# Kernel tuning notes

Hardware: AMD Instinct MI355X
Metric: run time of the kernel (lower is better)

Reference implementation:

```python
import jax, jax.numpy as jnp
import numpy as np

B, T, H, IN = 256, 1024, 512, 1

def setup_inputs() -> dict:
    key = jax.random.key(0)
    ks = jax.random.split(key, 10)
    s = 1.0 / np.sqrt(H)
    return {
        "input": jax.random.normal(ks[0], (B, T), dtype=jnp.float32),
        "Wx0": jax.random.uniform(ks[1], (IN, 4 * H), jnp.float32, -s, s),
        "Wh0": jax.random.uniform(ks[2], (H, 4 * H), jnp.float32, -s, s),
        "b0": jax.random.uniform(ks[3], (4 * H,), jnp.float32, -s, s),
        "Wx1": jax.random.uniform(ks[4], (H, 4 * H), jnp.float32, -s, s),
        "Wh1": jax.random.uniform(ks[5], (H, 4 * H), jnp.float32, -s, s),
        "b1": jax.random.uniform(ks[6], (4 * H,), jnp.float32, -s, s),
        "Wf": jax.random.uniform(ks[7], (H, 1), jnp.float32, -s, s),
        "bf": jax.random.uniform(ks[8], (1,), jnp.float32, -s, s),
    }

def _lstm_layer(xs, Wx, Wh, b):
    # xs: [T, B, in] -> hs: [T, B, H]
    Bd = xs.shape[1]
    Hd = Wh.shape[0]
    h0 = jnp.zeros((Bd, Hd), xs.dtype)
    c0 = jnp.zeros((Bd, Hd), xs.dtype)
    def step(carry, x_t):
        h, c = carry
        g = x_t @ Wx + h @ Wh + b                     # [B, 4H]
        i, f, gg, o = jnp.split(g, 4, axis=-1)
        i = jax.nn.sigmoid(i)
        f = jax.nn.sigmoid(f)
        gg = jnp.tanh(gg)
        o = jax.nn.sigmoid(o)
        c_n = f * c + i * gg
        h_n = o * jnp.tanh(c_n)
        return (h_n, c_n), h_n
    _, hs = jax.lax.scan(step, (h0, c0), xs)
    return hs

def reference(input, Wx0, Wh0, b0, Wx1, Wh1, b1, Wf, bf):
    # input: [B, T] scalar sequence (input_size = 1)
    xs = input.T[:, :, None]                           # [T, B, 1]
    h1 = _lstm_layer(xs, Wx0, Wh0, b0)                 # [T, B, H]
    h2 = _lstm_layer(h1, Wx1, Wh1, b1)                 # [T, B, H]
    out = h2 @ Wf + bf                                 # [T, B, 1]
    return out[:, :, 0].T                              # [B, T]
```

## Files before the change

### kernel.cpp

```cpp
#include <hip/hip_runtime.h>


typedef _Float16 f16;
typedef _Float16 f16x8 __attribute__((ext_vector_type(8)));
typedef float f32x4 __attribute__((ext_vector_type(4)));
typedef unsigned long long u64;

#define NB 256
#define NT_ 1024
#define NH 512
#define RING 16
#define SLOT (NB * NH)

__device__ __forceinline__ float sigm(float x)  { return 1.0f / (1.0f + __expf(-x)); }
__device__ __forceinline__ float tanhx(float x) { return 2.0f / (1.0f + __expf(-2.0f * x)) - 1.0f; }

__device__ __forceinline__ void st8(unsigned short* p, u64 v) {
  __hip_atomic_store((u64*)p, v, __ATOMIC_RELAXED, __HIP_MEMORY_SCOPE_AGENT);
}
__device__ __forceinline__ void stf(unsigned* p, unsigned v) {
  __hip_atomic_store(p, v, __ATOMIC_RELAXED, __HIP_MEMORY_SCOPE_AGENT);
}
__device__ __forceinline__ unsigned ldf(const unsigned* p) {
  return __hip_atomic_load(p, __ATOMIC_RELAXED, __HIP_MEMORY_SCOPE_AGENT);
}
__device__ __forceinline__ unsigned pollr(const unsigned* a, unsigned thr) {
  unsigned v;
  for (;;) {
    v = ldf(a);
    if (!~__ballot(v >= thr)) break;
    __builtin_amdgcn_s_sleep(1);
  }
  asm volatile("" ::: "memory");
  return v;
}

__device__ __forceinline__ unsigned* PFL(unsigned* pf, int c, int j, int r) {
  return pf + (((c * 16 + j) * 4) + r) * 32;
}
__device__ __forceinline__ unsigned* QFL(unsigned* qf, int c, int j, int r) {
  return qf + (((c * 32 + j) * 4) + r) * 32;
}

__global__ void prep_xT(const float* __restrict__ inp, float* __restrict__ xT) {
  int g = blockIdx.x * 256 + threadIdx.x;
  int t = g >> 8, b = g & 255;
  xT[t * NB + b] = inp[b * NT_ + t];
}

__global__ void prep_w(const float* __restrict__ Wh0,
                       const float* __restrict__ Wx1,
                       const float* __restrict__ Wh1,
                       f16* __restrict__ dst) {
  int g = blockIdx.x * 256 + threadIdx.x;
  int mat = g >> 20;
  int r = g & 0xFFFFF;
  int j = r & 7, ln = (r >> 3) & 63, kt = (r >> 9) & 15;
  int cl = ln & 15, qd = ln >> 4;
  int k = kt * 32 + qd * 8 + j;
  size_t di; int gcol; const float* W;
  if (mat == 0) {
    int gt = (r >> 13) & 3, nh = (r >> 15) & 1, sl = (r >> 16) & 15;
    W = Wh0;
    gcol = gt * 512 + sl * 32 + nh * 16 + cl;
    di = (size_t)sl * 65536 + (((size_t)(nh * 4 + gt) * 16 + kt) * 64 + ln) * 8 + j;
  } else {
    int jt = (r >> 13) & 1, nh = (r >> 14) & 1, sl = (r >> 15) & 31;
    W = (mat == 1) ? Wx1 : Wh1;
    int gate = jt * 2 + (cl >> 3);
    gcol = gate * 512 + sl * 16 + nh * 8 + (cl & 7);
    di = (size_t)mat * 1048576 + (size_t)sl * 32768 +
         (((size_t)(nh * 2 + jt) * 16 + kt) * 64 + ln) * 8 + j;
  }
  dst[di] = (f16)W[(size_t)k * 2048 + gcol];
}

__global__ void reduce_out(const float* __restrict__ part8,
                           const float* __restrict__ bfp,
                           float* __restrict__ out) {
  int g = blockIdx.x * 256 + threadIdx.x;
  float v = bfp[0];
#pragma unroll
  for (int j = 0; j < 8; ++j) v += part8[(size_t)j * (NB * NT_) + g];
  out[g] = v;
}

__global__ __launch_bounds__(256, 1) void lstm_main(
    const float* __restrict__ xT,
    const f16*  __restrict__ wsl,
    const float* __restrict__ wx0,
    const float* __restrict__ bias0,
    const float* __restrict__ bias1,
    const float* __restrict__ wf,
    unsigned short* p_hi, unsigned short* p_lo,
    unsigned short* q_hi, unsigned short* q_lo,
    unsigned int* pf,
    unsigned int* qf,
    float* part8)
{
  extern __shared__ char smem[];
  const int tid = threadIdx.x;
  const int wv = tid >> 6, ln = tid & 63;
  const int qd = ln >> 4, cl = ln & 15;
  const int bx = blockIdx.x;
  const int r8 = bx & 7, idx = bx >> 3;
  const bool isL0 = !(r8 & 1);
  const int c = r8 >> 1;
  const int sl = idx;
  if (isL0 && idx >= 16) return;
  const float LO = 1.0f / 1024.0f;

  if (isL0) {
    const int4* s0 = (const int4*)wsl + (size_t)sl * 8192;
    int4* d = (int4*)smem;
    for (int i = tid; i < 8192; i += 256) d[i] = s0[i];
  } else {
    const int4* s1 = (const int4*)wsl + 131072 + (size_t)sl * 4096;
    const int4* s2 = (const int4*)wsl + 262144 + (size_t)sl * 4096;
    int4* d = (int4*)smem;
    for (int i = tid; i < 4096; i += 256) { d[i] = s1[i]; d[4096 + i] = s2[i]; }
  }
  __syncthreads();

  if (isL0) {
    const int nh = wv >> 1, rhalf = wv & 1;
    const int rb0 = c * 64 + rhalf * 32;
    float wx0v[4], b0c[4];
#pragma unroll
    for (int g = 0; g < 4; ++g) {
      int gc = g * 512 + sl * 32 + nh * 16 + cl;
      wx0v[g] = wx0[gc];
      b0c[g] = bias0[gc];
    }
    float cst[2][4] = {{0.f,0.f,0.f,0.f},{0.f,0.f,0.f,0.f}};
    const bool isq = (ln >= 16 && ln < 48);
    const unsigned* pwa;
    if (ln < 16)      pwa = PFL(pf, c, ln, sl & 3);
    else if (ln < 48) pwa = QFL(qf, c, ln - 16, sl & 3);
    else              pwa = PFL(pf, c, ln - 48, (sl + 1) & 3);
    const f16x8* wl = (const f16x8*)smem;
    f16* sh  = (f16*)(smem + 131072);
    f16* slo = sh + 2048;

    for (int s = 0; s < NT_; ++s) {
      if ((s & (RING - 1)) == 0 && s) {
        __syncthreads();
        if (wv == 0)
          asm volatile("buffer_inv sc1\n\ts_waitcnt vmcnt(0)" ::: "memory");
        __syncthreads();
      }
      const int slot_r = (s + RING - 1) & (RING - 1);
      const int slot_w = s & (RING - 1);
      float4 xv[2];
#pragma unroll
      for (int rt = 0; rt < 2; ++rt)
        xv[rt] = *(const float4*)(xT + s * NB + rb0 + rt * 16 + qd * 4);
      if (s) {
        unsigned thr = isq ? (s >= RING ? (unsigned)(s - RING + 1) : 0u)
                           : (unsigned)s;
        pollr(pwa, thr);
      }
      f16x8 Ah[16][2], Al[16][2];
      {
        const f16* bh = (const f16*)p_hi + (size_t)slot_r * SLOT + (size_t)c * 32768 + qd * 8;
        const f16* bl = (const f16*)p_lo + (size_t)slot_r * SLOT + (size_t)c * 32768 + qd * 8;
#pragma unroll
        for (int kt = 0; kt < 16; ++kt)
#pragma unroll
          for (int rt = 0; rt < 2; ++rt) {
            int lr = rhalf * 32 + rt * 16 + cl;
            size_t off = (size_t)kt * 2048 + lr * 32;
            Ah[kt][rt] = *(const f16x8*)(bh + off);
            Al[kt][rt] = *(const f16x8*)(bl + off);
          }
      }
      f32x4 acc[4][2], accL[4][2];
#pragma unroll
      for (int g = 0; g < 4; ++g)
#pragma unroll
        for (int rt = 0; rt < 2; ++rt) {
          acc[g][rt] = (f32x4){0.f,0.f,0.f,0.f};
          accL[g][rt] = (f32x4){0.f,0.f,0.f,0.f};
        }
#pragma unroll
      for (int kt = 0; kt < 16; ++kt) {
#pragma unroll
        for (int g = 0; g < 4; ++g) {
          f16x8 bw = wl[((nh * 4 + g) * 16 + kt) * 64 + ln];
#pragma unroll
          for (int rt = 0; rt < 2; ++rt) {
            acc[g][rt]  = __builtin_amdgcn_mfma_f32_16x16x32_f16(Ah[kt][rt], bw, acc[g][rt], 0, 0, 0);
            accL[g][rt] = __builtin_amdgcn_mfma_f32_16x16x32_f16(Al[kt][rt], bw, accL[g][rt], 0, 0, 0);
          }
        }
      }
#pragma unroll
      for (int rt = 0; rt < 2; ++rt)
#pragma unroll
        for (int e = 0; e < 4; ++e) {
          float xe = (e == 0) ? xv[rt].x : (e == 1) ? xv[rt].y : (e == 2) ? xv[rt].z : xv[rt].w;
          float gi = acc[0][rt][e] + accL[0][rt][e] * LO + xe * wx0v[0] + b0c[0];
          float gf = acc[1][rt][e] + accL[1][rt][e] * LO + xe * wx0v[1] + b0c[1];
          float gg = acc[2][rt][e] + accL[2][rt][e] * LO + xe * wx0v[2] + b0c[2];
          float go = acc[3][rt][e] + accL[3][rt][e] * LO + xe * wx0v[3] + b0c[3];
          float ii = sigm(gi), ff = sigm(gf), tg = tanhx(gg), oo = sigm(go);
          cst[rt][e] = ff * cst[rt][e] + ii * tg;
          float h = oo * tanhx(cst[rt][e]);
          f16 hh = (f16)h;
          int su = (rhalf * 32 + rt * 16 + qd * 4 + e) * 32 + nh * 16 + cl;
          sh[su]  = hh;
          slo[su] = (f16)((h - (float)hh) * 1024.0f);
        }
      __syncthreads();
      {
        unsigned short* bh = p_hi + (size_t)slot_w * SLOT + (size_t)c * 32768 + (size_t)sl * 2048;
        unsigned short* bl = p_lo + (size_t)slot_w * SLOT + (size_t)c * 32768 + (size_t)sl * 2048;
#pragma unroll
        for (int i = tid; i < 1024; i += 256) {
          int strm = i >> 9, pc = i & 511;
          const f16* src = (strm ? slo : sh) + pc * 4;
          st8((strm ? bl : bh) + pc * 4, *(const u64*)src);
        }
      }
      __syncthreads();
      if (tid < 4)
        stf(PFL(pf, c, sl, tid), (unsigned)(s + 1));
    }
  } else {
    int u = cl & 7, g01 = cl >> 3;
    const bool hiH = (cl < 8);
    float b1c0[2], b1c1[2], wfv[2];
#pragma unroll
    for (int nh = 0; nh < 2; ++nh) {
      int base = sl * 16 + nh * 8 + u;
      b1c0[nh] = bias1[g01 * 512 + base];
      b1c1[nh] = bias1[(2 + g01) * 512 + base];
      wfv[nh] = wf[base];
    }
    const int lr = wv * 16 + cl;
    float cst[2][4] = {{0.f,0.f,0.f,0.f},{0.f,0.f,0.f,0.f}};
    const unsigned* a_init;
    const bool isPf = (ln >= 32 && ln < 48);
    if (ln < 32)      a_init = QFL(qf, c, ln, sl & 3);
    else if (ln < 48) a_init = PFL(pf, c, ln - 32, sl & 3);
    else              a_init = QFL(qf, c, ln - 48, (sl + 1) & 3);
    const unsigned* ppf = PFL(pf, c, ln & 15, (sl + (ln >> 4)) & 3);
    const f16x8* wx_ = (const f16x8*)smem;
    const f16x8* wh_ = (const f16x8*)(smem + 65536);
    f16* sh  = (f16*)(smem + 131072);
    f16* slo = sh + 1024;

    for (int s = 0; s < NT_; ++s) {
      if ((s & (RING - 1)) == 0 && s) {
        __syncthreads();
        if (wv == 0)
          asm volatile("buffer_inv sc1\n\ts_waitcnt vmcnt(0)" ::: "memory");
        __syncthreads();
      }
      const int slot_r = (s + RING - 1) & (RING - 1);
      const int slot_w = s & (RING - 1);
      bool early = false;
      if (s) {
        unsigned thr_i = isPf ? (unsigned)(s + 1) : (unsigned)s;
        unsigned v = ldf(a_init);
        u64 bal = __ballot(v >= thr_i);
        while ((unsigned)bal != 0xFFFFFFFFu) {
          __builtin_amdgcn_s_sleep(1);
          v = ldf(a_init);
          bal = __ballot(v >= thr_i);
        }
        asm volatile("" ::: "memory");
        early = (((bal >> 32) & 0xFFFF) == 0xFFFF);
      }
      const f16* aqh = (const f16*)q_hi + (size_t)slot_r * SLOT + (size_t)c * 32768 +
                       (qd >> 1) * 1024 + lr * 16 + (qd & 1) * 8;
      const f16* aql = (const f16*)q_lo + (size_t)slot_r * SLOT + (size_t)c * 32768 +
                       (qd >> 1) * 1024 + lr * 16 + (qd & 1) * 8;
      f16x8 Aq[16][2];
#pragma unroll
      for (int kt = 0; kt < 16; ++kt) {
        Aq[kt][0] = *(const f16x8*)(aqh + kt * 2048);
        Aq[kt][1] = *(const f16x8*)(aql + kt * 2048);
      }
      const f16* aph = (const f16*)p_hi + (size_t)slot_w * SLOT + (size_t)c * 32768 +
                       lr * 32 + qd * 8;
      const f16* apl = (const f16*)p_lo + (size_t)slot_w * SLOT + (size_t)c * 32768 +
                       lr * 32 + qd * 8;
      f16x8 Ap[16][2];
      if (early) {
#pragma unroll
        for (int kt = 0; kt < 16; ++kt) {
          Ap[kt][0] = *(const f16x8*)(aph + kt * 2048);
          Ap[kt][1] = *(const f16x8*)(apl + kt * 2048);
        }
      }
      f32x4 acc[4], accL[4];
#pragma unroll
      for (int t4 = 0; t4 < 4; ++t4) {
        acc[t4] = (f32x4){0.f,0.f,0.f,0.f};
        accL[t4] = (f32x4){0.f,0.f,0.f,0.f};
      }
#pragma unroll
      for (int kt = 0; kt < 16; ++kt) {
#pragma unroll
        for (int t4 = 0; t4 < 4; ++t4) {
          f16x8 bw = wh_[(t4 * 16 + kt) * 64 + ln];
          acc[t4]  = __builtin_amdgcn_mfma_f32_16x16x32_f16(Aq[kt][0], bw, acc[t4], 0, 0, 0);
          accL[t4] = __builtin_amdgcn_mfma_f32_16x16x32_f16(Aq[kt][1], bw, accL[t4], 0, 0, 0);
        }
      }
      if (!early) {
        pollr(ppf, (unsigned)(s + 1));
#pragma unroll
        for (int kt = 0; kt < 16; ++kt) {
          Ap[kt][0] = *(const f16x8*)(aph + kt * 2048);
          Ap[kt][1] = *(const f16x8*)(apl + kt * 2048);
        }
      }
#pragma unroll
      for (int kt = 0; kt < 16; ++kt) {
#pragma unroll
        for (int t4 = 0; t4 < 4; ++t4) {
          f16x8 bw = wx_[(t4 * 16 + kt) * 64 + ln];
          acc[t4]  = __builtin_amdgcn_mfma_f32_16x16x32_f16(Ap[kt][0], bw, acc[t4], 0, 0, 0);
          accL[t4] = __builtin_amdgcn_mfma_f32_16x16x32_f16(Ap[kt][1], bw, accL[t4], 0, 0, 0);
        }
      }
      float po[4];
#pragma unroll
      for (int e = 0; e < 4; ++e) {
        po[e] = 0.0f;
#pragma unroll
        for (int nh = 0; nh < 2; ++nh) {
          float v0 = acc[nh*2+0][e] + accL[nh*2+0][e] * LO + b1c0[nh];
          float v1 = acc[nh*2+1][e] + accL[nh*2+1][e] * LO + b1c1[nh];
          float w0 = __shfl_xor(v0, 8, 16);
          float w1 = __shfl_xor(v1, 8, 16);
          float gi = hiH ? v0 : w0;
          float gf = hiH ? w0 : v0;
          float gg = hiH ? v1 : w1;
          float go = hiH ? w1 : v1;
          float ii = sigm(gi), ff = sigm(gf), tg = tanhx(gg), oo = sigm(go);
          cst[nh][e] = ff * cst[nh][e] + ii * tg;
          float h = oo * tanhx(cst[nh][e]);
          int su = (wv * 16 + qd * 4 + e) * 16 + nh * 8 + u;
          if (hiH) {
            sh[su] = (f16)h;
          } else {
            f16 hh = (f16)h;
            slo[su] = (f16)((h - (float)hh) * 1024.0f);
          }
          po[e] += hiH ? wfv[nh] * h : 0.0f;
        }
      }
      __syncthreads();
      {
        unsigned short* bhq = q_hi + (size_t)slot_w * SLOT + (size_t)c * 32768 + (size_t)sl * 1024;
        unsigned short* blq = q_lo + (size_t)slot_w * SLOT + (size_t)c * 32768 + (size_t)sl * 1024;
#pragma unroll
        for (int i = tid; i < 512; i += 256) {
          int strm = i >> 8, pc = i & 255;
          const f16* src = (strm ? slo : sh) + pc * 4;
          st8((strm ? blq : bhq) + pc * 4, *(const u64*)src);
        }
      }
      __syncthreads();
      if (tid < 4)
        stf(QFL(qf, c, sl, tid), (unsigned)(s + 1));
#pragma unroll
      for (int e = 0; e < 4; ++e) {
        float r = po[e];
#pragma unroll
        for (int m = 1; m < 16; m <<= 1) r += __shfl_xor(r, m, 16);
        if (cl == 0)
          atomicAdd(part8 + (size_t)(sl & 7) * (NB * NT_) +
                        (size_t)(c * 64 + wv * 16 + qd * 4 + e) * NT_ + s, r);
      }
    }
  }
}

extern "C" void kernel_launch(void* const* d_in, const int* in_sizes, int n_in,
                              void* d_out, int out_size, void* d_ws, size_t ws_size,
                              hipStream_t stream) {
  (void)in_sizes; (void)n_in; (void)out_size; (void)ws_size;
  const float* inp = (const float*)d_in[0];
  const float* Wx0 = (const float*)d_in[1];
  const float* Wh0 = (const float*)d_in[2];
  const float* b0  = (const float*)d_in[3];
  const float* Wx1 = (const float*)d_in[4];
  const float* Wh1 = (const float*)d_in[5];
  const float* b1  = (const float*)d_in[6];
  const float* Wf  = (const float*)d_in[7];
  const float* bf  = (const float*)d_in[8];

  const size_t MB = 1u << 20;
  const size_t OFF_W    = 0;
  const size_t OFF_XT   = 6 * MB;
  const size_t OFF_PHI  = 7 * MB;
  const size_t OFF_PLO  = 11 * MB;
  const size_t OFF_QHI  = 15 * MB;
  const size_t OFF_QLO  = 19 * MB;
  const size_t OFF_PART = 23 * MB;
  const size_t OFF_CTR  = 31 * MB;

  char* ws = (char*)d_ws;
  f16* wsl = (f16*)(ws + OFF_W);
  float* xT = (float*)(ws + OFF_XT);
  unsigned short* phi = (unsigned short*)(ws + OFF_PHI);
  unsigned short* plo = (unsigned short*)(ws + OFF_PLO);
  unsigned short* qhi = (unsigned short*)(ws + OFF_QHI);
  unsigned short* qlo = (unsigned short*)(ws + OFF_QLO);
  float* part8 = (float*)(ws + OFF_PART);
  unsigned int* pfl = (unsigned int*)(ws + OFF_CTR);
  unsigned int* qfl = pfl + 8192;
  float* out = (float*)d_out;

  (void)hipFuncSetAttribute((const void*)lstm_main,
                            hipFuncAttributeMaxDynamicSharedMemorySize, 139264);

  (void)hipMemsetAsync(ws + OFF_PHI, 0, (OFF_CTR + 98304) - OFF_PHI, stream);

  prep_xT<<<1024, 256, 0, stream>>>(inp, xT);
  prep_w<<<12288, 256, 0, stream>>>(Wh0, Wx1, Wh1, wsl);

  lstm_main<<<256, 256, 139264, stream>>>(xT, wsl, Wx0, b0, b1, Wf,
                                          phi, plo, qhi, qlo, pfl, qfl, part8);

  reduce_out<<<1024, 256, 0, stream>>>(part8, bf, out);
}
```

Baseline: 10.21 ms.

## Split layer-0 LSTM across 32 slices per batch chunk instead of 16

```diff
diff --git a/kernel.cpp b/kernel.cpp
--- a/kernel.cpp
+++ b/kernel.cpp
@@ -36,7 +36,7 @@
 }
 
 __device__ __forceinline__ unsigned* PFL(unsigned* pf, int c, int j, int r) {
-  return pf + (((c * 16 + j) * 4) + r) * 32;
+  return pf + (((c * 32 + j) * 4) + r) * 32;
 }
 __device__ __forceinline__ unsigned* QFL(unsigned* qf, int c, int j, int r) {
   return qf + (((c * 32 + j) * 4) + r) * 32;
@@ -58,20 +58,12 @@
   int j = r & 7, ln = (r >> 3) & 63, kt = (r >> 9) & 15;
   int cl = ln & 15, qd = ln >> 4;
   int k = kt * 32 + qd * 8 + j;
-  size_t di; int gcol; const float* W;
-  if (mat == 0) {
-    int gt = (r >> 13) & 3, nh = (r >> 15) & 1, sl = (r >> 16) & 15;
-    W = Wh0;
-    gcol = gt * 512 + sl * 32 + nh * 16 + cl;
-    di = (size_t)sl * 65536 + (((size_t)(nh * 4 + gt) * 16 + kt) * 64 + ln) * 8 + j;
-  } else {
-    int jt = (r >> 13) & 1, nh = (r >> 14) & 1, sl = (r >> 15) & 31;
-    W = (mat == 1) ? Wx1 : Wh1;
-    int gate = jt * 2 + (cl >> 3);
-    gcol = gate * 512 + sl * 16 + nh * 8 + (cl & 7);
-    di = (size_t)mat * 1048576 + (size_t)sl * 32768 +
-         (((size_t)(nh * 2 + jt) * 16 + kt) * 64 + ln) * 8 + j;
-  }
+  int jt = (r >> 13) & 1, nh = (r >> 14) & 1, sl = (r >> 15) & 31;
+  const float* W = (mat == 0) ? Wh0 : (mat == 1) ? Wx1 : Wh1;
+  int gate = jt * 2 + (cl >> 3);
+  int gcol = gate * 512 + sl * 16 + nh * 8 + (cl & 7);
+  size_t di = (size_t)mat * 1048576 + (size_t)sl * 32768 +
+              (((size_t)(nh * 2 + jt) * 16 + kt) * 64 + ln) * 8 + j;
   dst[di] = (f16)W[(size_t)k * 2048 + gcol];
 }
 
@@ -107,13 +99,15 @@
   const bool isL0 = !(r8 & 1);
   const int c = r8 >> 1;
   const int sl = idx;
-  if (isL0 && idx >= 16) return;
   const float LO = 1.0f / 1024.0f;
+  const int u = cl & 7, g01 = cl >> 3;
+  const bool hiH = (cl < 8);
+  const int lr = wv * 16 + cl;
 
   if (isL0) {
-    const int4* s0 = (const int4*)wsl + (size_t)sl * 8192;
+    const int4* s0 = (const int4*)wsl + (size_t)sl * 4096;
     int4* d = (int4*)smem;
-    for (int i = tid; i < 8192; i += 256) d[i] = s0[i];
+    for (int i = tid; i < 4096; i += 256) d[i] = s0[i];
   } else {
     const int4* s1 = (const int4*)wsl + 131072 + (size_t)sl * 4096;
     const int4* s2 = (const int4*)wsl + 262144 + (size_t)sl * 4096;
@@ -123,24 +117,21 @@
   __syncthreads();
 
   if (isL0) {
-    const int nh = wv >> 1, rhalf = wv & 1;
-    const int rb0 = c * 64 + rhalf * 32;
-    float wx0v[4], b0c[4];
-#pragma unroll
-    for (int g = 0; g < 4; ++g) {
-      int gc = g * 512 + sl * 32 + nh * 16 + cl;
-      wx0v[g] = wx0[gc];
-      b0c[g] = bias0[gc];
+    float w0a[2], w0b[2], b0a[2], b0b[2];
+#pragma unroll
+    for (int nh = 0; nh < 2; ++nh) {
+      int base = sl * 16 + nh * 8 + u;
+      w0a[nh] = wx0[g01 * 512 + base];
+      b0a[nh] = bias0[g01 * 512 + base];
+      w0b[nh] = wx0[(2 + g01) * 512 + base];
+      b0b[nh] = bias0[(2 + g01) * 512 + base];
     }
     float cst[2][4] = {{0.f,0.f,0.f,0.f},{0.f,0.f,0.f,0.f}};
-    const bool isq = (ln >= 16 && ln < 48);
-    const unsigned* pwa;
-    if (ln < 16)      pwa = PFL(pf, c, ln, sl & 3);
-    else if (ln < 48) pwa = QFL(qf, c, ln - 16, sl & 3);
-    else              pwa = PFL(pf, c, ln - 48, (sl + 1) & 3);
+    const unsigned* pwa = (ln < 32) ? PFL(pf, c, ln, sl & 3)
+                                    : QFL(qf, c, ln - 32, sl & 3);
     const f16x8* wl = (const f16x8*)smem;
-    f16* sh  = (f16*)(smem + 131072);
-    f16* slo = sh + 2048;
+    f16* sh  = (f16*)(smem + 65536);
+    f16* slo = sh + 1024;
 
     for (int s = 0; s < NT_; ++s) {
       if ((s & (RING - 1)) == 0 && s) {
@@ -151,73 +142,70 @@
       }
       const int slot_r = (s + RING - 1) & (RING - 1);
       const int slot_w = s & (RING - 1);
-      float4 xv[2];
-#pragma unroll
-      for (int rt = 0; rt < 2; ++rt)
-        xv[rt] = *(const float4*)(xT + s * NB + rb0 + rt * 16 + qd * 4);
+      float4 xv = *(const float4*)(xT + s * NB + c * 64 + wv * 16 + qd * 4);
       if (s) {
-        unsigned thr = isq ? (s >= RING ? (unsigned)(s - RING + 1) : 0u)
-                           : (unsigned)s;
+        unsigned thr = (ln < 32) ? (unsigned)s
+                                 : (s >= RING ? (unsigned)(s - RING + 1) : 0u);
         pollr(pwa, thr);
       }
-      f16x8 Ah[16][2], Al[16][2];
-      {
-        const f16* bh = (const f16*)p_hi + (size_t)slot_r * SLOT + (size_t)c * 32768 + qd * 8;
-        const f16* bl = (const f16*)p_lo + (size_t)slot_r * SLOT + (size_t)c * 32768 + qd * 8;
-#pragma unroll
-        for (int kt = 0; kt < 16; ++kt)
-#pragma unroll
-          for (int rt = 0; rt < 2; ++rt) {
-            int lr = rhalf * 32 + rt * 16 + cl;
-            size_t off = (size_t)kt * 2048 + lr * 32;
-            Ah[kt][rt] = *(const f16x8*)(bh + off);
-            Al[kt][rt] = *(const f16x8*)(bl + off);
+      const f16* ah = (const f16*)p_hi + (size_t)slot_r * SLOT + (size_t)c * 32768 +
+                      (qd >> 1) * 1024 + lr * 16 + (qd & 1) * 8;
+      const f16* al = (const f16*)p_lo + (size_t)slot_r * SLOT + (size_t)c * 32768 +
+                      (qd >> 1) * 1024 + lr * 16 + (qd & 1) * 8;
+      f16x8 Ah[16], Al[16];
+#pragma unroll
+      for (int kt = 0; kt < 16; ++kt) {
+        Ah[kt] = *(const f16x8*)(ah + kt * 2048);
+        Al[kt] = *(const f16x8*)(al + kt * 2048);
+      }
+      f32x4 acc[4], accL[4];
+#pragma unroll
+      for (int t4 = 0; t4 < 4; ++t4) {
+        acc[t4] = (f32x4){0.f,0.f,0.f,0.f};
+        accL[t4] = (f32x4){0.f,0.f,0.f,0.f};
+      }
+#pragma unroll
+      for (int kt = 0; kt < 16; ++kt) {
+#pragma unroll
+        for (int t4 = 0; t4 < 4; ++t4) {
+          f16x8 bw = wl[(t4 * 16 + kt) * 64 + ln];
+          acc[t4]  = __builtin_amdgcn_mfma_f32_16x16x32_f16(Ah[kt], bw, acc[t4], 0, 0, 0);
+          accL[t4] = __builtin_amdgcn_mfma_f32_16x16x32_f16(Al[kt], bw, accL[t4], 0, 0, 0);
+        }
+      }
+#pragma unroll
+      for (int e = 0; e < 4; ++e) {
+        float xe = (e == 0) ? xv.x : (e == 1) ? xv.y : (e == 2) ? xv.z : xv.w;
+        int r = wv * 16 + qd * 4 + e;
+#pragma unroll
+        for (int nh = 0; nh < 2; ++nh) {
+          float v0 = acc[nh*2+0][e] + accL[nh*2+0][e] * LO + xe * w0a[nh] + b0a[nh];
+          float v1 = acc[nh*2+1][e] + accL[nh*2+1][e] * LO + xe * w0b[nh] + b0b[nh];
+          float w0 = __shfl_xor(v0, 8, 16);
+          float w1 = __shfl_xor(v1, 8, 16);
+          float gi = hiH ? v0 : w0;
+          float gf = hiH ? w0 : v0;
+          float gg = hiH ? v1 : w1;
+          float go = hiH ? w1 : v1;
+          float ii = sigm(gi), ff = sigm(gf), tg = tanhx(gg), oo = sigm(go);
+          cst[nh][e] = ff * cst[nh][e] + ii * tg;
+          float h = oo * tanhx(cst[nh][e]);
+          int su = r * 16 + nh * 8 + u;
+          if (hiH) {
+            sh[su] = (f16)h;
+          } else {
+            f16 hh = (f16)h;
+            slo[su] = (f16)((h - (float)hh) * 1024.0f);
           }
-      }
-      f32x4 acc[4][2], accL[4][2];
-#pragma unroll
-      for (int g = 0; g < 4; ++g)
-#pragma unroll
-        for (int rt = 0; rt < 2; ++rt) {
-          acc[g][rt] = (f32x4){0.f,0.f,0.f,0.f};
-          accL[g][rt] = (f32x4){0.f,0.f,0.f,0.f};
-        }
-#pragma unroll
-      for (int kt = 0; kt < 16; ++kt) {
-#pragma unroll
-        for (int g = 0; g < 4; ++g) {
-          f16x8 bw = wl[((nh * 4 + g) * 16 + kt) * 64 + ln];
-#pragma unroll
-          for (int rt = 0; rt < 2; ++rt) {
-            acc[g][rt]  = __builtin_amdgcn_mfma_f32_16x16x32_f16(Ah[kt][rt], bw, acc[g][rt], 0, 0, 0);
-            accL[g][rt] = __builtin_amdgcn_mfma_f32_16x16x32_f16(Al[kt][rt], bw, accL[g][rt], 0, 0, 0);
-          }
-        }
-      }
-#pragma unroll
-      for (int rt = 0; rt < 2; ++rt)
-#pragma unroll
-        for (int e = 0; e < 4; ++e) {
-          float xe = (e == 0) ? xv[rt].x : (e == 1) ? xv[rt].y : (e == 2) ? xv[rt].z : xv[rt].w;
-          float gi = acc[0][rt][e] + accL[0][rt][e] * LO + xe * wx0v[0] + b0c[0];
-          float gf = acc[1][rt][e] + accL[1][rt][e] * LO + xe * wx0v[1] + b0c[1];
-          float gg = acc[2][rt][e] + accL[2][rt][e] * LO + xe * wx0v[2] + b0c[2];
-          float go = acc[3][rt][e] + accL[3][rt][e] * LO + xe * wx0v[3] + b0c[3];
-          float ii = sigm(gi), ff = sigm(gf), tg = tanhx(gg), oo = sigm(go);
-          cst[rt][e] = ff * cst[rt][e] + ii * tg;
-          float h = oo * tanhx(cst[rt][e]);
-          f16 hh = (f16)h;
-          int su = (rhalf * 32 + rt * 16 + qd * 4 + e) * 32 + nh * 16 + cl;
-          sh[su]  = hh;
-          slo[su] = (f16)((h - (float)hh) * 1024.0f);
-        }
+        }
+      }
       __syncthreads();
       {
-        unsigned short* bh = p_hi + (size_t)slot_w * SLOT + (size_t)c * 32768 + (size_t)sl * 2048;
-        unsigned short* bl = p_lo + (size_t)slot_w * SLOT + (size_t)c * 32768 + (size_t)sl * 2048;
-#pragma unroll
-        for (int i = tid; i < 1024; i += 256) {
-          int strm = i >> 9, pc = i & 511;
+        unsigned short* bh = p_hi + (size_t)slot_w * SLOT + (size_t)c * 32768 + (size_t)sl * 1024;
+        unsigned short* bl = p_lo + (size_t)slot_w * SLOT + (size_t)c * 32768 + (size_t)sl * 1024;
+#pragma unroll
+        for (int i = tid; i < 512; i += 256) {
+          int strm = i >> 8, pc = i & 255;
           const f16* src = (strm ? slo : sh) + pc * 4;
           st8((strm ? bl : bh) + pc * 4, *(const u64*)src);
         }
@@ -227,8 +215,6 @@
         stf(PFL(pf, c, sl, tid), (unsigned)(s + 1));
     }
   } else {
-    int u = cl & 7, g01 = cl >> 3;
-    const bool hiH = (cl < 8);
     float b1c0[2], b1c1[2], wfv[2];
 #pragma unroll
     for (int nh = 0; nh < 2; ++nh) {
@@ -237,14 +223,10 @@
       b1c1[nh] = bias1[(2 + g01) * 512 + base];
       wfv[nh] = wf[base];
     }
-    const int lr = wv * 16 + cl;
     float cst[2][4] = {{0.f,0.f,0.f,0.f},{0.f,0.f,0.f,0.f}};
-    const unsigned* a_init;
-    const bool isPf = (ln >= 32 && ln < 48);
-    if (ln < 32)      a_init = QFL(qf, c, ln, sl & 3);
-    else if (ln < 48) a_init = PFL(pf, c, ln - 32, sl & 3);
-    else              a_init = QFL(qf, c, ln - 48, (sl + 1) & 3);
-    const unsigned* ppf = PFL(pf, c, ln & 15, (sl + (ln >> 4)) & 3);
+    const unsigned* a_init = (ln < 32) ? QFL(qf, c, ln, sl & 3)
+                                       : PFL(pf, c, ln - 32, sl & 3);
+    const unsigned* ppf = PFL(pf, c, ln & 31, (sl + (ln >> 5)) & 3);
     const f16x8* wx_ = (const f16x8*)smem;
     const f16x8* wh_ = (const f16x8*)(smem + 65536);
     f16* sh  = (f16*)(smem + 131072);
@@ -261,7 +243,7 @@
       const int slot_w = s & (RING - 1);
       bool early = false;
       if (s) {
-        unsigned thr_i = isPf ? (unsigned)(s + 1) : (unsigned)s;
+        unsigned thr_i = (ln < 32) ? (unsigned)s : (unsigned)(s + 1);
         unsigned v = ldf(a_init);
         u64 bal = __ballot(v >= thr_i);
         while ((unsigned)bal != 0xFFFFFFFFu) {
@@ -270,7 +252,7 @@
           bal = __ballot(v >= thr_i);
         }
         asm volatile("" ::: "memory");
-        early = (((bal >> 32) & 0xFFFF) == 0xFFFF);
+        early = ((unsigned)(bal >> 32) == 0xFFFFFFFFu);
       }
       const f16* aqh = (const f16*)q_hi + (size_t)slot_r * SLOT + (size_t)c * 32768 +
                        (qd >> 1) * 1024 + lr * 16 + (qd & 1) * 8;
@@ -283,9 +265,9 @@
         Aq[kt][1] = *(const f16x8*)(aql + kt * 2048);
       }
       const f16* aph = (const f16*)p_hi + (size_t)slot_w * SLOT + (size_t)c * 32768 +
-                       lr * 32 + qd * 8;
+                       (qd >> 1) * 1024 + lr * 16 + (qd & 1) * 8;
       const f16* apl = (const f16*)p_lo + (size_t)slot_w * SLOT + (size_t)c * 32768 +
-                       lr * 32 + qd * 8;
+                       (qd >> 1) * 1024 + lr * 16 + (qd & 1) * 8;
       f16x8 Ap[16][2];
       if (early) {
 #pragma unroll
@@ -413,18 +395,18 @@
   unsigned short* qlo = (unsigned short*)(ws + OFF_QLO);
   float* part8 = (float*)(ws + OFF_PART);
   unsigned int* pfl = (unsigned int*)(ws + OFF_CTR);
-  unsigned int* qfl = pfl + 8192;
+  unsigned int* qfl = pfl + 16384;
   float* out = (float*)d_out;
 
   (void)hipFuncSetAttribute((const void*)lstm_main,
-                            hipFuncAttributeMaxDynamicSharedMemorySize, 139264);
-
-  (void)hipMemsetAsync(ws + OFF_PHI, 0, (OFF_CTR + 98304) - OFF_PHI, stream);
+                            hipFuncAttributeMaxDynamicSharedMemorySize, 135168);
+
+  (void)hipMemsetAsync(ws + OFF_PHI, 0, (OFF_CTR + 131072) - OFF_PHI, stream);
 
   prep_xT<<<1024, 256, 0, stream>>>(inp, xT);
   prep_w<<<12288, 256, 0, stream>>>(Wh0, Wx1, Wh1, wsl);
 
-  lstm_main<<<256, 256, 139264, stream>>>(xT, wsl, Wx0, b0, b1, Wf,
+  lstm_main<<<256, 256, 135168, stream>>>(xT, wsl, Wx0, b0, b1, Wf,
                                           phi, plo, qhi, qlo, pfl, qfl, part8);
 
   reduce_out<<<1024, 256, 0, stream>>>(part8, bf, out);
```

New measurement: 9.664 ms. 5.3% less time.
